# Kernel optimization log

Measured on AMD Instinct MI355X. Metric: run time of the kernel, lower is better.

Reference implementation:

```python
import jax, jax.numpy as jnp
import numpy as np

N, H, LAT, V = 256, 450, 56, 780  # nodes, hidden_size, latent_size, vocab_size


def _build_tree(seed=0):
    """Random tree on N nodes + DFS path matching the torch dfs() (children in ascending id order)."""
    rng = np.random.default_rng(seed)
    children = [[] for _ in range(N)]
    for i in range(1, N):
        children[int(rng.integers(0, i))].append(i)
    path = []
    stack = [(0, 0)]
    while stack:
        u, ci = stack.pop()
        ch = children[u]
        if ci < len(ch):
            stack.append((u, ci + 1))
            path.append((u, 1))   # descend to child -> stop flag 1
            stack.append((ch[ci], 0))
        else:
            path.append((u, 0))   # backtrack -> stop flag 0
    return path


def setup_inputs() -> dict:
    key = jax.random.key(0)
    ks = jax.random.split(key, 18)
    path = _build_tree()
    L = len(path)  # 2N-1 = 511
    node_ids = np.array([p[0] for p in path], dtype=np.int32)
    stops = np.array([p[1] for p in path], dtype=np.int32)
    next_ids = np.concatenate([node_ids[1:], np.zeros(1, np.int32)])
    label_steps = np.where(stops == 1)[0].astype(np.int32)  # N-1 steps that emit a label
    rng = np.random.default_rng(1)
    vids = rng.integers(0, V, size=N).astype(np.int32)
    node_feature = np.zeros((N, V), np.float32)
    node_feature[np.arange(N), vids] = 1.0  # one-hot vocab features, as in JT-VAE
    real_labels = np.concatenate([vids[:1], vids[next_ids[label_steps]]]).astype(np.int32)  # [N]
    w = lambda k, shape: (jax.random.normal(k, shape, jnp.float32) * 0.05)
    return {
        "latent_code": jax.random.normal(ks[0], (LAT,), jnp.float32),
        "node_feature": jnp.asarray(node_feature),
        "node_ids": jnp.asarray(node_ids),
        "next_ids": jnp.asarray(next_ids),
        "stops": jnp.asarray(stops),
        "label_steps": jnp.asarray(label_steps),
        "real_labels": jnp.asarray(real_labels),
        "Wz_w": w(ks[1], (H, V + H)), "Wz_b": w(ks[2], (H,)),
        "Ur_w": w(ks[3], (H, H)),
        "Wr_w": w(ks[4], (H, V)), "Wr_b": w(ks[5], (H,)),
        "Wh_w": w(ks[6], (H, V + H)), "Wh_b": w(ks[7], (H,)),
        "Wd12_w": w(ks[8], (H, V + LAT)), "Wd12_b": w(ks[9], (H,)),
        "Wd3_w": w(ks[10], (H, H)), "Wd3_b": w(ks[11], (H,)),
        "Ud_w": w(ks[12], (1, 2 * H)), "Ud_b": w(ks[13], (1,)),
        "Wl_w": w(ks[14], (H, H + LAT)), "Wl_b": w(ks[15], (H,)),
        "Ul_w": w(ks[16], (V, H)), "Ul_b": w(ks[17], (V,)),
    }


def reference(latent_code, node_feature, node_ids, next_ids, stops, label_steps, real_labels,
              Wz_w, Wz_b, Ur_w, Wr_w, Wr_b, Wh_w, Wh_b, Wd12_w, Wd12_b, Wd3_w, Wd3_b,
              Ud_w, Ud_b, Wl_w, Wl_b, Ul_w, Ul_b):
    n = node_feature.shape[0]
    h = Wz_w.shape[0]
    L = node_ids.shape[0]

    # Root label: F.relu(U_l(W_l(cat(latent, zeros(h)))))  -- relu OUTSIDE U_l, no softmax.
    root_in = jnp.concatenate([latent_code, jnp.zeros((h,), latent_code.dtype)])
    root_label = jax.nn.relu((root_in @ Wl_w.T + Wl_b) @ Ul_w.T + Ul_b)

    def step(carry, xs):
        hidden, enc = carry            # hidden: [n,n,h], enc: [n,n]
        a, b, is_last = xs
        x = node_feature[a]            # [V] one-hot row
        hs = hidden[:, a]              # [n,h] incoming messages into node a
        # Stop prediction (uses pre-update hidden)
        d12 = jnp.concatenate([x, latent_code]) @ Wd12_w.T + Wd12_b
        d3 = hs.sum(0) @ Wd3_w.T + Wd3_b
        pred_stop = (jax.nn.relu(jnp.concatenate([d12, d3])) @ Ud_w.T + Ud_b)[0]
        # GRU message a -> b, excluding the edge (a,b) from the neighbor mask
        enc0 = enc.at[a, b].set(0.0).at[b, a].set(0.0)
        mask = enc0[:, a]              # [n]
        Hm = hs * mask[:, None]        # masked gathered hidden
        s = Hm.sum(0)                  # [h]
        z = jax.nn.sigmoid(jnp.concatenate([x, s]) @ Wz_w.T + Wz_b)
        r1 = x @ Wr_w.T + Wr_b         # [h]
        r = jax.nn.sigmoid(r1 + Hm @ Ur_w.T)  # [n,h]; torch sums sigmoid over ALL n rows
        gated = jnp.tanh(jnp.concatenate([x, r.sum(0)]) @ Wh_w.T + Wh_b)
        new_h = (1.0 - z) * s + z * gated
        hidden_new = hidden.at[a, b].set(new_h)
        enc_new = enc0.at[a, b].set(1.0).at[b, a].set(1.0)
        hidden = jnp.where(is_last, hidden, hidden_new)  # last path entry: break before update
        enc = jnp.where(is_last, enc, enc_new)
        # Child label: softmax(U_l(relu(W_l(cat(latent, new_h)))))  -- relu INSIDE, then softmax
        lab_in = jnp.concatenate([latent_code, new_h])
        label = jax.nn.softmax(jax.nn.relu(lab_in @ Wl_w.T + Wl_b) @ Ul_w.T + Ul_b)
        return (hidden, enc), (pred_stop, label)

    hidden0 = jnp.zeros((n, n, h), jnp.float32)
    enc0 = jnp.zeros((n, n), jnp.float32)
    is_last = jnp.arange(L) == (L - 1)
    (_, _), (pred_stops, labels) = jax.lax.scan(step, (hidden0, enc0), (node_ids, next_ids, is_last))
    pred_labels = jnp.concatenate([root_label[None], labels[label_steps]], axis=0)  # [N, V]
    return stops.astype(jnp.float32), pred_stops, real_labels, pred_labels
```

## Files before the change

### kernel.cpp

```cpp
#include <hip/hip_runtime.h>
#include <math.h>

#define NN   256
#define HH   450
#define LATD 56
#define VV   780
#define LL   511
#define GSEQ 32
#define TSEQ 512
#define KMAX 15
#define AST  16
#define RING 8

__device__ __forceinline__ float wred_sum(float v) {
    for (int off = 32; off; off >>= 1) v += __shfl_down(v, off, 64);
    return v;
}

__device__ __forceinline__ void barrier_lds() {
    asm volatile("s_waitcnt lgkmcnt(0)" ::: "memory");
    __builtin_amdgcn_s_barrier();
}

__device__ __forceinline__ void ast64(unsigned long long* p, unsigned long long v) {
    __hip_atomic_store(p, v, __ATOMIC_RELAXED, __HIP_MEMORY_SCOPE_AGENT);
}
__device__ __forceinline__ unsigned long long ald64(const unsigned long long* p) {
    return __hip_atomic_load(p, __ATOMIC_RELAXED, __HIP_MEMORY_SCOPE_AGENT);
}
__device__ __forceinline__ unsigned long long pk64(float v, unsigned tag) {
    return ((unsigned long long)tag << 32) | (unsigned long long)__float_as_uint(v);
}
__device__ __forceinline__ float lo32f(unsigned long long x) { return __uint_as_float((unsigned)x); }
__device__ __forceinline__ unsigned hi32(unsigned long long x) { return (unsigned)(x >> 32); }

__device__ __forceinline__ float poll4(const unsigned long long* pp, unsigned tag) {
    unsigned long long a = ald64(pp);
    if (hi32(a) == tag) return lo32f(a);
    unsigned long long b = ald64(pp);
    unsigned long long c = ald64(pp);
    unsigned long long d = ald64(pp);
    for (;;) {
        if (hi32(a) == tag) return lo32f(a);
        a = b; b = c; c = d; d = ald64(pp);
    }
}

__global__ void k_vid(const float* __restrict__ nf, int* __restrict__ vid) {
    const int u = blockIdx.x;
    for (int v = threadIdx.x; v < VV; v += blockDim.x)
        if (nf[(size_t)u * VV + v] > 0.5f) vid[u] = v;
}

__global__ __launch_bounds__(512) void k_consts(
    const int* __restrict__ vid, const float* __restrict__ latent,
    const float* __restrict__ Wz, const float* __restrict__ Wzb,
    const float* __restrict__ Wr, const float* __restrict__ Wrb,
    const float* __restrict__ Wh, const float* __restrict__ Whb,
    const float* __restrict__ Wd12, const float* __restrict__ Wd12b,
    const float* __restrict__ Ud,
    float* __restrict__ cz, float* __restrict__ r1s, float* __restrict__ sig0,
    float* __restrict__ ch, float* __restrict__ dotd12)
{
    const int u = blockIdx.x, tid = threadIdx.x;
    const int v = vid[u];
    __shared__ float red[8];
    float p = 0.f;
    if (tid < HH) {
        const int i = tid, o = u * HH + i;
        cz[o] = Wz[(size_t)i * (VV + HH) + v] + Wzb[i];
        const float r1 = Wr[(size_t)i * VV + v] + Wrb[i];
        r1s[o] = r1;
        sig0[o] = 1.f / (1.f + expf(-r1));
        ch[o] = Wh[(size_t)i * (VV + HH) + v] + Whb[i];
        float d = Wd12[(size_t)i * (VV + LATD) + v] + Wd12b[i];
        for (int k = 0; k < LATD; ++k)
            d += Wd12[(size_t)i * (VV + LATD) + VV + k] * latent[k];
        p = Ud[i] * fmaxf(d, 0.f);
    }
    p = wred_sum(p);
    if ((tid & 63) == 0) red[tid >> 6] = p;
    __syncthreads();
    if (tid == 0) {
        float s = 0.f;
        for (int w = 0; w < 8; ++w) s += red[w];
        dotd12[u] = s;
    }
}

__global__ __launch_bounds__(512) void k_whsig0(
    const float* __restrict__ Wh, const float* __restrict__ sig0, float* __restrict__ out)
{
    const int u = blockIdx.x, tid = threadIdx.x, wave = tid >> 6, lane = tid & 63;
    __shared__ float sg[HH];
    if (tid < HH) sg[tid] = sig0[u * HH + tid];
    __syncthreads();
    for (int r = wave; r < HH; r += 8) {
        float acc = 0.f;
        for (int k = lane; k < HH; k += 64)
            acc += Wh[(size_t)r * (VV + HH) + VV + k] * sg[k];
        acc = wred_sum(acc);
        if (lane == 0) out[u * HH + r] = acc;
    }
}

__global__ void k_excl(const int* __restrict__ node_ids, const int* __restrict__ next_ids,
                       int* __restrict__ excl, float* __restrict__ ccpre)
{
    const int t = blockIdx.x;
    __shared__ int ex, cnt;
    if (threadIdx.x == 0) { ex = -1; cnt = 0; }
    __syncthreads();
    const int a = node_ids[t], b = next_ids[t];
    for (int tp = threadIdx.x; tp <= t; tp += blockDim.x) {
        if (tp < t && node_ids[tp] == b && next_ids[tp] == a) ex = tp;
        if (tp >= 1 && node_ids[tp] == a) atomicAdd(&cnt, 1);
    }
    __syncthreads();
    if (threadIdx.x == 0) {
        excl[t] = ex;
        ccpre[t] = 256.f - (float)cnt + (ex >= 0 ? 1.f : 0.f);
    }
}

__global__ void k_copy(const int* __restrict__ stops, const int* __restrict__ reall,
                       float* __restrict__ out)
{
    const int i = blockIdx.x * blockDim.x + threadIdx.x;
    if (i < LL) { out[i] = (float)stops[i]; out[LL + i] = 0.f; }
    if (i < NN) out[2 * LL + i] = (float)reall[i];
}

__global__ void k_pred(const float* __restrict__ pred_part, float* __restrict__ out) {
    const int t = blockIdx.x * blockDim.x + threadIdx.x;
    if (t < LL) {
        float s = 0.f;
        #pragma unroll 8
        for (int b = 0; b < GSEQ; ++b) s += pred_part[(size_t)t * GSEQ + b];
        out[LL + t] = s;
    }
}

#define KEEP16(w) asm volatile("" : \
    "+v"(w[0]), "+v"(w[1]), "+v"(w[2]),  "+v"(w[3]),  "+v"(w[4]),  "+v"(w[5]),  "+v"(w[6]),  "+v"(w[7]), \
    "+v"(w[8]), "+v"(w[9]), "+v"(w[10]), "+v"(w[11]), "+v"(w[12]), "+v"(w[13]), "+v"(w[14]), "+v"(w[15]))

__global__ __launch_bounds__(TSEQ, 1) void k_seq(
    const int* __restrict__ node_ids, const int* __restrict__ excl,
    const float* __restrict__ ccpre,
    const float* __restrict__ Ur, const float* __restrict__ Wz,
    const float* __restrict__ Wh, const float* __restrict__ Wd3,
    const float* __restrict__ Wd3b, const float* __restrict__ Ud,
    const float* __restrict__ Udb,
    const float* __restrict__ cz, const float* __restrict__ r1s,
    const float* __restrict__ ch, const float* __restrict__ WhSig0,
    const float* __restrict__ dotd12,
    float* __restrict__ NewHL, float* __restrict__ WzML, float* __restrict__ WhSvL,
    unsigned long long* __restrict__ bcNh, unsigned long long* __restrict__ bcSig,
    float* __restrict__ pred_part)
{
    const int tid = threadIdx.x, bid = blockIdx.x;
    const int wave = tid >> 6, lane = tid & 63;
    const int kcnt = 14 + (bid < 2 ? 1 : 0);
    const int kbeg = 14 * bid + (bid < 2 ? bid : 2);

    float* myNewH = NewHL  + (size_t)bid * LL * AST;
    float* myWzM  = WzML   + (size_t)bid * LL * AST;
    float* myWhSv = WhSvL  + (size_t)bid * LL * AST;

    __shared__ float sSm[NN * AST];
    __shared__ float sWzSm[NN * AST];
    __shared__ float sWhRs[NN * AST];
    __shared__ float sWd3S[NN * AST];
    __shared__ float nh_full[512];
    __shared__ float sig_full[512];
    __shared__ float sNhR[RING][AST];
    __shared__ float sWzR[RING][AST];
    __shared__ float sWhR[RING][AST];

    float urw[16], wzw[16], wd3w[16], whw[16];
    #pragma unroll
    for (int it = 0; it < 2; ++it) {
        const int j = wave + 8 * it;
        const bool vj = j < kcnt;
        const int r = vj ? (kbeg + j) : 0;
        #pragma unroll
        for (int e = 0; e < 8; ++e) {
            const int c = lane + 64 * e;
            const bool vc = vj && (c < HH);
            urw[it * 8 + e]  = vc ? Ur[(size_t)r * HH + c] : 0.f;
            wzw[it * 8 + e]  = vc ? Wz[(size_t)r * (VV + HH) + VV + c] : 0.f;
            wd3w[it * 8 + e] = vc ? Wd3[(size_t)r * HH + c] : 0.f;
            whw[it * 8 + e]  = vc ? Wh[(size_t)r * (VV + HH) + VV + c] : 0.f;
        }
    }
    KEEP16(urw); KEEP16(wzw); KEEP16(wd3w); KEEP16(whw);

    float ud_r = 0.f, w3b_r = 0.f;
    if (tid < kcnt) { ud_r = Ud[HH + kbeg + tid]; w3b_r = Wd3b[kbeg + tid]; }
    const float udb0 = Udb[0];

    for (int i = tid; i < NN * AST; i += TSEQ) {
        sSm[i] = 0.f; sWzSm[i] = 0.f; sWhRs[i] = 0.f; sWd3S[i] = 0.f;
    }
    nh_full[tid] = 0.f; sig_full[tid] = 0.f;

    int ap = node_ids[0];
    float pcz = 0.f, pch = 0.f, pws = 0.f;
    if (tid < kcnt) {
        const int o = ap * HH + kbeg + tid;
        pcz = cz[o]; pch = ch[o]; pws = WhSig0[o];
    }
    float pcc = ccpre[0];
    int  pidx = excl[0];
    float pe_nh = 0.f, pe_wz = 0.f, pe_wh = 0.f;
    const bool own_row = tid >= kbeg && tid < kbeg + kcnt;
    __syncthreads();

    for (int t = 1; t <= LL; ++t) {
        const int idx = pidx;
        float nh = 0.f;
        if (tid < kcnt) {
            const int oa = ap * AST + tid;
            float zarg = sWzSm[oa] + pcz;
            float whv  = sWhRs[oa] + pch;
            float sv   = sSm[oa];
            if (idx >= 0) {
                float enh, ewz, ewh;
                if (idx >= t - RING) {
                    const int sl = idx & (RING - 1);
                    enh = sNhR[sl][tid]; ewz = sWzR[sl][tid]; ewh = sWhR[sl][tid];
                } else {
                    enh = pe_nh; ewz = pe_wz; ewh = pe_wh;
                }
                zarg -= ewz; whv -= ewh; sv -= enh;
            }
            whv += pcc * pws;
            const float z = 1.f / (1.f + expf(-zarg));
            nh = (1.f - z) * sv + z * tanhf(whv);
            if (t < LL) {
                ast64(&bcNh[(size_t)((t & 1) * 512 + kbeg + tid)], pk64(nh, (unsigned)t));
                nh_full[kbeg + tid] = nh;
            }
            myNewH[(t - 1) * AST + tid] = nh;
            sNhR[(t - 1) & (RING - 1)][tid] = nh;
        }
        if (wave == 0) {
            float ps = 0.f;
            if (tid < kcnt)
                ps = ud_r * fmaxf(sWd3S[ap * AST + tid] + w3b_r, 0.f);
            ps = wred_sum(ps);
            if (lane == 0) {
                if (bid == 0) ps += dotd12[ap] + udb0;
                pred_part[(size_t)(t - 1) * GSEQ + bid] = ps;
            }
        }
        if (t == LL) break;
        const int a = node_ids[t];
        const unsigned tag = (unsigned)t;
        const int p = t & 1;

        pidx = excl[t];
        pe_nh = pe_wz = pe_wh = 0.f;
        if (pidx >= 0 && pidx < t - (RING - 1) && tid < kcnt) {
            const int oe = pidx * AST + tid;
            pe_nh = myNewH[oe]; pe_wz = myWzM[oe]; pe_wh = myWhSv[oe];
        }
        float r1v[2];
        #pragma unroll
        for (int it = 0; it < 2; ++it) {
            const int j = wave + 8 * it;
            r1v[it] = r1s[(size_t)a * HH + ((j < kcnt) ? (kbeg + j) : 0)];
        }
        float ncz = 0.f, nch = 0.f, nws = 0.f;
        if (tid < kcnt) {
            const int o = a * HH + kbeg + tid;
            ncz = cz[o]; nch = ch[o]; nws = WhSig0[o];
        }
        const float ncc = ccpre[t];
        if (tid < kcnt) sSm[a * AST + tid] += nh;

        if (tid < HH && !own_row)
            nh_full[tid] = poll4(&bcNh[(size_t)(p * 512 + tid)], tag);
        barrier_lds();

        #pragma unroll
        for (int it = 0; it < 2; ++it) {
            const int j = wave + 8 * it;
            float acc = 0.f;
            #pragma unroll
            for (int e = 0; e < 8; ++e) acc += urw[it * 8 + e] * nh_full[lane + 64 * e];
            acc = wred_sum(acc);
            if (lane == 0 && j < kcnt) {
                const float sg = 1.f / (1.f + expf(-(acc + r1v[it])));
                ast64(&bcSig[(size_t)(p * 512 + kbeg + j)], pk64(sg, tag));
                sig_full[kbeg + j] = sg;
            }
        }

        #pragma unroll
        for (int it = 0; it < 2; ++it) {
            const int j = wave + 8 * it;
            float az = 0.f, ad = 0.f;
            #pragma unroll
            for (int e = 0; e < 8; ++e) {
                const float x = nh_full[lane + 64 * e];
                az += wzw[it * 8 + e] * x;
                ad += wd3w[it * 8 + e] * x;
            }
            az = wred_sum(az); ad = wred_sum(ad);
            if (lane == 0 && j < kcnt) {
                myWzM[(t - 1) * AST + j] = az;
                sWzR[(t - 1) & (RING - 1)][j] = az;
                sWzSm[a * AST + j] += az;
                sWd3S[a * AST + j] += ad;
            }
        }
        pcz = ncz; pch = nch; pws = nws; pcc = ncc;

        if (tid < HH && !own_row)
            sig_full[tid] = poll4(&bcSig[(size_t)(p * 512 + tid)], tag);
        barrier_lds();

        #pragma unroll
        for (int it = 0; it < 2; ++it) {
            const int j = wave + 8 * it;
            float aw = 0.f;
            #pragma unroll
            for (int e = 0; e < 8; ++e) aw += whw[it * 8 + e] * sig_full[lane + 64 * e];
            aw = wred_sum(aw);
            if (lane == 0 && j < kcnt) {
                myWhSv[(t - 1) * AST + j] = aw;
                sWhR[(t - 1) & (RING - 1)][j] = aw;
                sWhRs[a * AST + j] += aw;
            }
        }
        ap = a;
        barrier_lds();
    }
}

__global__ __launch_bounds__(512) void k_label(
    const float* __restrict__ latent, const int* __restrict__ lsteps,
    const float* __restrict__ NewHL,
    const float* __restrict__ Wl, const float* __restrict__ Wlb,
    const float* __restrict__ Ul, const float* __restrict__ Ulb,
    float* __restrict__ out)
{
    const int q = blockIdx.x, tid = threadIdx.x, wave = tid >> 6, lane = tid & 63;
    __shared__ float inp[LATD + HH];
    __shared__ float t2[HH];
    __shared__ float lg[VV];
    __shared__ float red[8];
    if (tid < LATD) inp[tid] = latent[tid];
    if (q == 0) {
        if (tid < HH) inp[LATD + tid] = 0.f;
    } else {
        const int t = lsteps[q - 1];
        if (tid < HH) {
            const int b = (tid < 30) ? (tid / 15) : (2 + (tid - 30) / 14);
            const int j = (tid < 30) ? (tid % 15) : ((tid - 30) % 14);
            inp[LATD + tid] = NewHL[((size_t)b * LL + t) * AST + j];
        }
    }
    __syncthreads();
    for (int r = wave; r < HH; r += 8) {
        float acc = 0.f;
        for (int k = lane; k < LATD + HH; k += 64)
            acc += Wl[(size_t)r * (LATD + HH) + k] * inp[k];
        acc = wred_sum(acc);
        if (lane == 0) {
            const float v = acc + Wlb[r];
            t2[r] = (q == 0) ? v : fmaxf(v, 0.f);
        }
    }
    __syncthreads();
    for (int r = wave; r < VV; r += 8) {
        float acc = 0.f;
        for (int k = lane; k < HH; k += 64) acc += Ul[(size_t)r * HH + k] * t2[k];
        acc = wred_sum(acc);
        if (lane == 0) lg[r] = acc + Ulb[r];
    }
    __syncthreads();
    float* outrow = out + 2 * LL + NN + (size_t)q * VV;
    if (q == 0) {
        for (int i = tid; i < VV; i += 512) outrow[i] = fmaxf(lg[i], 0.f);
        return;
    }
    float mx = -1e30f;
    for (int i = tid; i < VV; i += 512) mx = fmaxf(mx, lg[i]);
    for (int off = 32; off; off >>= 1) mx = fmaxf(mx, __shfl_down(mx, off, 64));
    if (lane == 0) red[wave] = mx;
    __syncthreads();
    if (tid == 0) {
        float m = red[0];
        for (int w = 1; w < 8; ++w) m = fmaxf(m, red[w]);
        red[0] = m;
    }
    __syncthreads();
    const float M = red[0];
    float sum = 0.f;
    for (int i = tid; i < VV; i += 512) { const float e = expf(lg[i] - M); lg[i] = e; sum += e; }
    __syncthreads();
    sum = wred_sum(sum);
    if (lane == 0) red[wave] = sum;
    __syncthreads();
    if (tid == 0) {
        float s = 0.f;
        for (int w = 0; w < 8; ++w) s += red[w];
        red[0] = s;
    }
    __syncthreads();
    const float S = red[0];
    for (int i = tid; i < VV; i += 512) outrow[i] = lg[i] / S;
}

extern "C" void kernel_launch(void* const* d_in, const int* in_sizes, int n_in,
                              void* d_out, int out_size, void* d_ws, size_t ws_size,
                              hipStream_t stream)
{
    const float* latent = (const float*)d_in[0];
    const float* nodef  = (const float*)d_in[1];
    const int* node_ids = (const int*)d_in[2];
    const int* next_ids = (const int*)d_in[3];
    const int* stops    = (const int*)d_in[4];
    const int* lsteps   = (const int*)d_in[5];
    const int* reall    = (const int*)d_in[6];
    const float* Wz   = (const float*)d_in[7];
    const float* Wzb  = (const float*)d_in[8];
    const float* Urw  = (const float*)d_in[9];
    const float* Wr   = (const float*)d_in[10];
    const float* Wrb  = (const float*)d_in[11];
    const float* Wh   = (const float*)d_in[12];
    const float* Whb  = (const float*)d_in[13];
    const float* Wd12 = (const float*)d_in[14];
    const float* Wd12b= (const float*)d_in[15];
    const float* Wd3  = (const float*)d_in[16];
    const float* Wd3b = (const float*)d_in[17];
    const float* Ud   = (const float*)d_in[18];
    const float* Udb  = (const float*)d_in[19];
    const float* Wl   = (const float*)d_in[20];
    const float* Wlb  = (const float*)d_in[21];
    const float* Ul   = (const float*)d_in[22];
    const float* Ulb  = (const float*)d_in[23];
    (void)in_sizes; (void)n_in; (void)out_size; (void)ws_size;
    float* out = (float*)d_out;
    float* W = (float*)d_ws;

    size_t o = 0;
    unsigned long long* bcNh  = (unsigned long long*)(W + o); o += 2 * 512 * 2;
    unsigned long long* bcSig = (unsigned long long*)(W + o); o += 2 * 512 * 2;
    const size_t zero_floats = o;
    int*   vid    = (int*)(W + o); o += NN;
    int*   excl   = (int*)(W + o); o += LL + 1;
    float* ccpre  = W + o; o += LL + 1;
    float* cz     = W + o; o += NN * HH;
    float* r1s    = W + o; o += NN * HH;
    float* sig0   = W + o; o += NN * HH;
    float* ch     = W + o; o += NN * HH;
    float* WhSig0 = W + o; o += NN * HH;
    float* dotd12 = W + o; o += NN;
    float* NewHL  = W + o; o += (size_t)GSEQ * LL * AST;
    float* WzML   = W + o; o += (size_t)GSEQ * LL * AST;
    float* WhSvL  = W + o; o += (size_t)GSEQ * LL * AST;
    float* predp  = W + o; o += (size_t)LL * GSEQ;

    hipMemsetAsync(W, 0, zero_floats * sizeof(float), stream);
    k_vid   <<<NN, 256, 0, stream>>>(nodef, vid);
    k_consts<<<NN, 512, 0, stream>>>(vid, latent, Wz, Wzb, Wr, Wrb, Wh, Whb,
                                     Wd12, Wd12b, Ud, cz, r1s, sig0, ch, dotd12);
    k_whsig0<<<NN, 512, 0, stream>>>(Wh, sig0, WhSig0);
    k_excl  <<<LL, 256, 0, stream>>>(node_ids, next_ids, excl, ccpre);
    k_copy  <<<2, 256, 0, stream>>>(stops, reall, out);
    k_seq   <<<GSEQ, TSEQ, 0, stream>>>(node_ids, excl, ccpre, Urw, Wz, Wh, Wd3, Wd3b,
                                        Ud, Udb, cz, r1s, ch, WhSig0, dotd12,
                                        NewHL, WzML, WhSvL,
                                        bcNh, bcSig,
                                        predp);
    k_pred  <<<1, 512, 0, stream>>>(predp, out);
    k_label <<<NN, 512, 0, stream>>>(latent, lsteps, NewHL, Wl, Wlb, Ul, Ulb, out);
}
```

Baseline: 2.283 ms.

## Restructure sequential step: early prefetch, batched sig broadcast, fast math, rotated polling

Moves the next step's global loads (node ids, exclusion index, precomputed constants, spilled history) to the top of the loop so they overlap with the current step's compute. Sigmoid values are first written to LDS, then broadcast by the owning threads in one coalesced store after a barrier, instead of lane 0 of each wave doing it. Global history writes are deferred and issued by the kcnt threads from the ring buffers. Polling thread indices are rotated so the wait load is spread differently, and the poll depth goes to 6 loads. Precise expf/tanhf are replaced with __expf-based versions, which are less accurate. It adds one extra barrier per step.

```diff
diff --git a/kernel.cpp b/kernel.cpp
--- a/kernel.cpp
+++ b/kernel.cpp
@@ -17,6 +17,16 @@
     return v;
 }
 
+__device__ __forceinline__ float fsig(float x) {
+    return 1.f / (1.f + __expf(-x));
+}
+__device__ __forceinline__ float ftanh(float x) {
+    const float t = fabsf(x);
+    const float e = __expf(-2.f * t);
+    const float r = (1.f - e) / (1.f + e);
+    return x < 0.f ? -r : r;
+}
+
 __device__ __forceinline__ void barrier_lds() {
     asm volatile("s_waitcnt lgkmcnt(0)" ::: "memory");
     __builtin_amdgcn_s_barrier();
@@ -34,15 +44,17 @@
 __device__ __forceinline__ float lo32f(unsigned long long x) { return __uint_as_float((unsigned)x); }
 __device__ __forceinline__ unsigned hi32(unsigned long long x) { return (unsigned)(x >> 32); }
 
-__device__ __forceinline__ float poll4(const unsigned long long* pp, unsigned tag) {
+__device__ __forceinline__ float poll6(const unsigned long long* pp, unsigned tag) {
     unsigned long long a = ald64(pp);
     if (hi32(a) == tag) return lo32f(a);
     unsigned long long b = ald64(pp);
     unsigned long long c = ald64(pp);
     unsigned long long d = ald64(pp);
+    unsigned long long e = ald64(pp);
+    unsigned long long f = ald64(pp);
     for (;;) {
         if (hi32(a) == tag) return lo32f(a);
-        a = b; b = c; c = d; d = ald64(pp);
+        a = b; b = c; c = d; d = e; e = f; f = ald64(pp);
     }
 }
 
@@ -163,6 +175,8 @@
     const int wave = tid >> 6, lane = tid & 63;
     const int kcnt = 14 + (bid < 2 ? 1 : 0);
     const int kbeg = 14 * bid + (bid < 2 ? bid : 2);
+    const int pw   = (kbeg + tid) & 511;
+    const bool do_poll = (tid >= kcnt) && (pw < HH);
 
     float* myNewH = NewHL  + (size_t)bid * LL * AST;
     float* myWzM  = WzML   + (size_t)bid * LL * AST;
@@ -214,10 +228,34 @@
     float pcc = ccpre[0];
     int  pidx = excl[0];
     float pe_nh = 0.f, pe_wz = 0.f, pe_wh = 0.f;
-    const bool own_row = tid >= kbeg && tid < kbeg + kcnt;
     __syncthreads();
 
     for (int t = 1; t <= LL; ++t) {
+        int a = 0, nidx = -1;
+        float r1v[2] = {0.f, 0.f};
+        float ncz = 0.f, nch = 0.f, nws = 0.f, ncc = 0.f;
+        float npe_nh = 0.f, npe_wz = 0.f, npe_wh = 0.f;
+        if (t < LL) {
+            a = node_ids[t];
+            nidx = excl[t];
+            if (nidx >= 0 && nidx < t - (RING - 1) && tid < kcnt) {
+                const int oe = nidx * AST + tid;
+                npe_nh = myNewH[oe]; npe_wz = myWzM[oe]; npe_wh = myWhSv[oe];
+            }
+            #pragma unroll
+            for (int it = 0; it < 2; ++it) {
+                const int j = wave + 8 * it;
+                r1v[it] = r1s[(size_t)a * HH + ((j < kcnt) ? (kbeg + j) : 0)];
+            }
+            if (tid < kcnt) {
+                const int o = a * HH + kbeg + tid;
+                ncz = cz[o]; nch = ch[o]; nws = WhSig0[o];
+            }
+            ncc = ccpre[t];
+        }
+        if (t >= 2 && tid < kcnt)
+            myWhSv[(size_t)(t - 2) * AST + tid] = sWhR[(t - 2) & (RING - 1)][tid];
+
         const int idx = pidx;
         float nh = 0.f;
         if (tid < kcnt) {
@@ -236,13 +274,13 @@
                 zarg -= ewz; whv -= ewh; sv -= enh;
             }
             whv += pcc * pws;
-            const float z = 1.f / (1.f + expf(-zarg));
-            nh = (1.f - z) * sv + z * tanhf(whv);
+            const float z = fsig(zarg);
+            nh = (1.f - z) * sv + z * ftanh(whv);
             if (t < LL) {
                 ast64(&bcNh[(size_t)((t & 1) * 512 + kbeg + tid)], pk64(nh, (unsigned)t));
                 nh_full[kbeg + tid] = nh;
             }
-            myNewH[(t - 1) * AST + tid] = nh;
+            myNewH[(size_t)(t - 1) * AST + tid] = nh;
             sNhR[(t - 1) & (RING - 1)][tid] = nh;
         }
         if (wave == 0) {
@@ -256,32 +294,15 @@
             }
         }
         if (t == LL) break;
-        const int a = node_ids[t];
         const unsigned tag = (unsigned)t;
         const int p = t & 1;
 
-        pidx = excl[t];
-        pe_nh = pe_wz = pe_wh = 0.f;
-        if (pidx >= 0 && pidx < t - (RING - 1) && tid < kcnt) {
-            const int oe = pidx * AST + tid;
-            pe_nh = myNewH[oe]; pe_wz = myWzM[oe]; pe_wh = myWhSv[oe];
-        }
-        float r1v[2];
-        #pragma unroll
-        for (int it = 0; it < 2; ++it) {
-            const int j = wave + 8 * it;
-            r1v[it] = r1s[(size_t)a * HH + ((j < kcnt) ? (kbeg + j) : 0)];
-        }
-        float ncz = 0.f, nch = 0.f, nws = 0.f;
-        if (tid < kcnt) {
-            const int o = a * HH + kbeg + tid;
-            ncz = cz[o]; nch = ch[o]; nws = WhSig0[o];
-        }
-        const float ncc = ccpre[t];
         if (tid < kcnt) sSm[a * AST + tid] += nh;
-
-        if (tid < HH && !own_row)
-            nh_full[tid] = poll4(&bcNh[(size_t)(p * 512 + tid)], tag);
+        pidx = nidx; pe_nh = npe_nh; pe_wz = npe_wz; pe_wh = npe_wh;
+        pcz = ncz; pch = nch; pws = nws; pcc = ncc;
+
+        if (do_poll)
+            nh_full[pw] = poll6(&bcNh[(size_t)(p * 512 + pw)], tag);
         barrier_lds();
 
         #pragma unroll
@@ -291,12 +312,14 @@
             #pragma unroll
             for (int e = 0; e < 8; ++e) acc += urw[it * 8 + e] * nh_full[lane + 64 * e];
             acc = wred_sum(acc);
-            if (lane == 0 && j < kcnt) {
-                const float sg = 1.f / (1.f + expf(-(acc + r1v[it])));
-                ast64(&bcSig[(size_t)(p * 512 + kbeg + j)], pk64(sg, tag));
-                sig_full[kbeg + j] = sg;
-            }
-        }
+            if (lane == 0 && j < kcnt)
+                sig_full[kbeg + j] = fsig(acc + r1v[it]);
+        }
+        barrier_lds();
+
+        if (tid < kcnt)
+            ast64(&bcSig[(size_t)(p * 512 + kbeg + tid)],
+                  pk64(sig_full[kbeg + tid], tag));
 
         #pragma unroll
         for (int it = 0; it < 2; ++it) {
@@ -310,17 +333,18 @@
             }
             az = wred_sum(az); ad = wred_sum(ad);
             if (lane == 0 && j < kcnt) {
-                myWzM[(t - 1) * AST + j] = az;
                 sWzR[(t - 1) & (RING - 1)][j] = az;
                 sWzSm[a * AST + j] += az;
                 sWd3S[a * AST + j] += ad;
             }
         }
-        pcz = ncz; pch = nch; pws = nws; pcc = ncc;
-
-        if (tid < HH && !own_row)
-            sig_full[tid] = poll4(&bcSig[(size_t)(p * 512 + tid)], tag);
+
+        if (do_poll)
+            sig_full[pw] = poll6(&bcSig[(size_t)(p * 512 + pw)], tag);
         barrier_lds();
+
+        if (tid < kcnt)
+            myWzM[(size_t)(t - 1) * AST + tid] = sWzR[(t - 1) & (RING - 1)][tid];
 
         #pragma unroll
         for (int it = 0; it < 2; ++it) {
@@ -330,7 +354,6 @@
             for (int e = 0; e < 8; ++e) aw += whw[it * 8 + e] * sig_full[lane + 64 * e];
             aw = wred_sum(aw);
             if (lane == 0 && j < kcnt) {
-                myWhSv[(t - 1) * AST + j] = aw;
                 sWhR[(t - 1) & (RING - 1)][j] = aw;
                 sWhRs[a * AST + j] += aw;
             }
```

New measurement: 2.481 ms. 1.09x slower.

## Halve sequential-kernel block count and switch to fast sigmoid/tanh

Applied to the files above, without the earlier changes.

Splits the hidden rows of the sequential recurrence kernel across 16 workgroups instead of 32, so each block holds 28-29 rows of weights in registers (NIT=4 row passes per wave) and LDS strides double. Fewer participants means fewer cross-block polls per step, at the price of more per-block matvec work each step. It also swaps expf/tanhf for __expf-based fast sigmoid and tanh, and deepens the polling pipeline from 4 to 6 outstanding loads. The label kernel's index mapping is updated to match the new partition.

```diff
diff --git a/kernel.cpp b/kernel.cpp
--- a/kernel.cpp
+++ b/kernel.cpp
@@ -6,10 +6,10 @@
 #define LATD 56
 #define VV   780
 #define LL   511
-#define GSEQ 32
+#define GSEQ 16
 #define TSEQ 512
-#define KMAX 15
-#define AST  16
+#define AST  32
+#define NIT  4
 #define RING 8
 
 __device__ __forceinline__ float wred_sum(float v) {
@@ -17,6 +17,16 @@
     return v;
 }
 
+__device__ __forceinline__ float fsig(float x) {
+    return 1.f / (1.f + __expf(-x));
+}
+__device__ __forceinline__ float ftanh(float x) {
+    const float t = fabsf(x);
+    const float e = __expf(-2.f * t);
+    const float r = (1.f - e) / (1.f + e);
+    return x < 0.f ? -r : r;
+}
+
 __device__ __forceinline__ void barrier_lds() {
     asm volatile("s_waitcnt lgkmcnt(0)" ::: "memory");
     __builtin_amdgcn_s_barrier();
@@ -34,15 +44,17 @@
 __device__ __forceinline__ float lo32f(unsigned long long x) { return __uint_as_float((unsigned)x); }
 __device__ __forceinline__ unsigned hi32(unsigned long long x) { return (unsigned)(x >> 32); }
 
-__device__ __forceinline__ float poll4(const unsigned long long* pp, unsigned tag) {
+__device__ __forceinline__ float poll6(const unsigned long long* pp, unsigned tag) {
     unsigned long long a = ald64(pp);
     if (hi32(a) == tag) return lo32f(a);
     unsigned long long b = ald64(pp);
     unsigned long long c = ald64(pp);
     unsigned long long d = ald64(pp);
+    unsigned long long e = ald64(pp);
+    unsigned long long f = ald64(pp);
     for (;;) {
         if (hi32(a) == tag) return lo32f(a);
-        a = b; b = c; c = d; d = ald64(pp);
+        a = b; b = c; c = d; d = e; e = f; f = ald64(pp);
     }
 }
 
@@ -142,8 +154,8 @@
 }
 
 #define KEEP16(w) asm volatile("" : \
-    "+v"(w[0]), "+v"(w[1]), "+v"(w[2]),  "+v"(w[3]),  "+v"(w[4]),  "+v"(w[5]),  "+v"(w[6]),  "+v"(w[7]), \
-    "+v"(w[8]), "+v"(w[9]), "+v"(w[10]), "+v"(w[11]), "+v"(w[12]), "+v"(w[13]), "+v"(w[14]), "+v"(w[15]))
+    "+v"((w)[0]), "+v"((w)[1]), "+v"((w)[2]),  "+v"((w)[3]),  "+v"((w)[4]),  "+v"((w)[5]),  "+v"((w)[6]),  "+v"((w)[7]), \
+    "+v"((w)[8]), "+v"((w)[9]), "+v"((w)[10]), "+v"((w)[11]), "+v"((w)[12]), "+v"((w)[13]), "+v"((w)[14]), "+v"((w)[15]))
 
 __global__ __launch_bounds__(TSEQ, 1) void k_seq(
     const int* __restrict__ node_ids, const int* __restrict__ excl,
@@ -161,8 +173,8 @@
 {
     const int tid = threadIdx.x, bid = blockIdx.x;
     const int wave = tid >> 6, lane = tid & 63;
-    const int kcnt = 14 + (bid < 2 ? 1 : 0);
-    const int kbeg = 14 * bid + (bid < 2 ? bid : 2);
+    const int kcnt = 28 + (bid < 2 ? 1 : 0);
+    const int kbeg = 28 * bid + (bid < 2 ? bid : 2);
 
     float* myNewH = NewHL  + (size_t)bid * LL * AST;
     float* myWzM  = WzML   + (size_t)bid * LL * AST;
@@ -178,9 +190,9 @@
     __shared__ float sWzR[RING][AST];
     __shared__ float sWhR[RING][AST];
 
-    float urw[16], wzw[16], wd3w[16], whw[16];
+    float urw[NIT * 8], wzw[NIT * 8], wd3w[NIT * 8], whw[NIT * 8];
     #pragma unroll
-    for (int it = 0; it < 2; ++it) {
+    for (int it = 0; it < NIT; ++it) {
         const int j = wave + 8 * it;
         const bool vj = j < kcnt;
         const int r = vj ? (kbeg + j) : 0;
@@ -194,7 +206,8 @@
             whw[it * 8 + e]  = vc ? Wh[(size_t)r * (VV + HH) + VV + c] : 0.f;
         }
     }
-    KEEP16(urw); KEEP16(wzw); KEEP16(wd3w); KEEP16(whw);
+    KEEP16(urw); KEEP16(urw + 16); KEEP16(wzw); KEEP16(wzw + 16);
+    KEEP16(wd3w); KEEP16(wd3w + 16); KEEP16(whw); KEEP16(whw + 16);
 
     float ud_r = 0.f, w3b_r = 0.f;
     if (tid < kcnt) { ud_r = Ud[HH + kbeg + tid]; w3b_r = Wd3b[kbeg + tid]; }
@@ -236,13 +249,13 @@
                 zarg -= ewz; whv -= ewh; sv -= enh;
             }
             whv += pcc * pws;
-            const float z = 1.f / (1.f + expf(-zarg));
-            nh = (1.f - z) * sv + z * tanhf(whv);
+            const float z = fsig(zarg);
+            nh = (1.f - z) * sv + z * ftanh(whv);
             if (t < LL) {
                 ast64(&bcNh[(size_t)((t & 1) * 512 + kbeg + tid)], pk64(nh, (unsigned)t));
                 nh_full[kbeg + tid] = nh;
             }
-            myNewH[(t - 1) * AST + tid] = nh;
+            myNewH[(size_t)(t - 1) * AST + tid] = nh;
             sNhR[(t - 1) & (RING - 1)][tid] = nh;
         }
         if (wave == 0) {
@@ -266,9 +279,9 @@
             const int oe = pidx * AST + tid;
             pe_nh = myNewH[oe]; pe_wz = myWzM[oe]; pe_wh = myWhSv[oe];
         }
-        float r1v[2];
+        float r1v[NIT];
         #pragma unroll
-        for (int it = 0; it < 2; ++it) {
+        for (int it = 0; it < NIT; ++it) {
             const int j = wave + 8 * it;
             r1v[it] = r1s[(size_t)a * HH + ((j < kcnt) ? (kbeg + j) : 0)];
         }
@@ -281,25 +294,25 @@
         if (tid < kcnt) sSm[a * AST + tid] += nh;
 
         if (tid < HH && !own_row)
-            nh_full[tid] = poll4(&bcNh[(size_t)(p * 512 + tid)], tag);
+            nh_full[tid] = poll6(&bcNh[(size_t)(p * 512 + tid)], tag);
         barrier_lds();
 
         #pragma unroll
-        for (int it = 0; it < 2; ++it) {
+        for (int it = 0; it < NIT; ++it) {
             const int j = wave + 8 * it;
             float acc = 0.f;
             #pragma unroll
             for (int e = 0; e < 8; ++e) acc += urw[it * 8 + e] * nh_full[lane + 64 * e];
             acc = wred_sum(acc);
             if (lane == 0 && j < kcnt) {
-                const float sg = 1.f / (1.f + expf(-(acc + r1v[it])));
+                const float sg = fsig(acc + r1v[it]);
                 ast64(&bcSig[(size_t)(p * 512 + kbeg + j)], pk64(sg, tag));
                 sig_full[kbeg + j] = sg;
             }
         }
 
         #pragma unroll
-        for (int it = 0; it < 2; ++it) {
+        for (int it = 0; it < NIT; ++it) {
             const int j = wave + 8 * it;
             float az = 0.f, ad = 0.f;
             #pragma unroll
@@ -310,7 +323,7 @@
             }
             az = wred_sum(az); ad = wred_sum(ad);
             if (lane == 0 && j < kcnt) {
-                myWzM[(t - 1) * AST + j] = az;
+                myWzM[(size_t)(t - 1) * AST + j] = az;
                 sWzR[(t - 1) & (RING - 1)][j] = az;
                 sWzSm[a * AST + j] += az;
                 sWd3S[a * AST + j] += ad;
@@ -319,18 +332,18 @@
         pcz = ncz; pch = nch; pws = nws; pcc = ncc;
 
         if (tid < HH && !own_row)
-            sig_full[tid] = poll4(&bcSig[(size_t)(p * 512 + tid)], tag);
+            sig_full[tid] = poll6(&bcSig[(size_t)(p * 512 + tid)], tag);
         barrier_lds();
 
         #pragma unroll
-        for (int it = 0; it < 2; ++it) {
+        for (int it = 0; it < NIT; ++it) {
             const int j = wave + 8 * it;
             float aw = 0.f;
             #pragma unroll
             for (int e = 0; e < 8; ++e) aw += whw[it * 8 + e] * sig_full[lane + 64 * e];
             aw = wred_sum(aw);
             if (lane == 0 && j < kcnt) {
-                myWhSv[(t - 1) * AST + j] = aw;
+                myWhSv[(size_t)(t - 1) * AST + j] = aw;
                 sWhR[(t - 1) & (RING - 1)][j] = aw;
                 sWhRs[a * AST + j] += aw;
             }
@@ -358,8 +371,8 @@
     } else {
         const int t = lsteps[q - 1];
         if (tid < HH) {
-            const int b = (tid < 30) ? (tid / 15) : (2 + (tid - 30) / 14);
-            const int j = (tid < 30) ? (tid % 15) : ((tid - 30) % 14);
+            const int b = (tid < 58) ? (tid / 29) : (2 + (tid - 58) / 28);
+            const int j = (tid < 58) ? (tid % 29) : ((tid - 58) % 28);
             inp[LATD + tid] = NewHL[((size_t)b * LL + t) * AST + j];
         }
     }
```

Measured after the change: 3.041 ms. +33.2%, slower.
